# Kernel tuning notes

Hardware: AMD Instinct MI355X
Metric: run time of the kernel (lower is better)

## Reference

```python
import jax, jax.numpy as jnp
import numpy as np

P = 1024          # nodes per graph
B = 64            # graphs in batch
N = P * B         # total nodes
E = N * 32        # total edges (avg degree 32)
D_IN = 16         # per-node feature dim (share_obs_dim)
H = 32            # GCN / MLP hidden dim (hardcoded in GNet)
SHARE = 64        # flat share_state dim


def setup_inputs() -> dict:
    key = jax.random.key(0)
    ks = jax.random.split(key, 20)

    x = jax.random.normal(ks[0], (N, D_IN), jnp.float32)
    src = jax.random.randint(ks[1], (E,), 0, N, dtype=jnp.int32)
    # keep edges inside each 1024-node graph block (PyG batched graphs)
    dst = (src // P) * P + jax.random.randint(ks[2], (E,), 0, P, dtype=jnp.int32)
    edge_index = jnp.stack([src, dst])
    value_batch = (jnp.arange(N, dtype=jnp.int32) // P)
    share_state = jax.random.normal(ks[3], (B, SHARE), jnp.float32)

    def lin(k, o, i):
        return jax.random.normal(k, (o, i), jnp.float32) / np.float32(np.sqrt(i))

    return {
        "x": x, "edge_index": edge_index, "value_batch": value_batch,
        "share_state": share_state,
        # value_gnet: GCNConv(D_IN,32), GCNConv(32,32), Linear(32,32), post-pool Linear(32,32)
        "W1": lin(ks[4], H, D_IN), "b1": jnp.zeros((H,), jnp.float32),
        "W2": lin(ks[5], H, H),    "b2": jnp.zeros((H,), jnp.float32),
        "Wl": lin(ks[6], H, H),    "bl": jnp.zeros((H,), jnp.float32),
        "Wp": lin(ks[7], H, H),    "bp": jnp.zeros((H,), jnp.float32),
        # value_net MLP: SHARE->32->32->32
        "Vw1": lin(ks[8], H, SHARE), "Vb1": jnp.zeros((H,), jnp.float32),
        "Vw2": lin(ks[9], H, H),     "Vb2": jnp.zeros((H,), jnp.float32),
        "Vw3": lin(ks[10], H, H),    "Vb3": jnp.zeros((H,), jnp.float32),
        # value_comnet: 64->32->1
        "Cw1": lin(ks[11], H, 2 * H), "Cb1": jnp.zeros((H,), jnp.float32),
        "Cw2": lin(ks[12], 1, H) * np.float32(0.01), "Cb2": jnp.zeros((1,), jnp.float32),
    }


def gcn_conv(x, src, dst, W, b):
    """PyG GCNConv: D^-1/2 (A+I) D^-1/2 X W^T + b (unit edge weights)."""
    n = x.shape[0]
    loop = jnp.arange(n, dtype=src.dtype)
    s = jnp.concatenate([src, loop])
    d = jnp.concatenate([dst, loop])
    deg = jax.ops.segment_sum(jnp.ones(s.shape[0], x.dtype), d, num_segments=n)
    dis = jnp.where(deg > 0, jax.lax.rsqrt(jnp.maximum(deg, 1e-12)), 0.0)
    norm = dis[s] * dis[d]                      # [E+N]
    h = x @ W.T                                  # [N, H] small GEMM first
    out = jax.ops.segment_sum(h[s] * norm[:, None], d, num_segments=n)
    return out + b


def reference(x, edge_index, value_batch, share_state,
              W1, b1, W2, b2, Wl, bl, Wp, bp,
              Vw1, Vb1, Vw2, Vb2, Vw3, Vb3,
              Cw1, Cb1, Cw2, Cb2):
    src, dst = edge_index[0], edge_index[1]
    nb = share_state.shape[0]

    # value_gnet
    h = jnp.tanh(gcn_conv(x, src, dst, W1, b1))
    h = jnp.tanh(gcn_conv(h, src, dst, W2, b2))
    h = jnp.tanh(h @ Wl.T + bl)
    pooled = jax.ops.segment_sum(h, value_batch, num_segments=nb)  # global_add_pool -> [B, 32]
    h1 = pooled @ Wp.T + bp

    # value_net MLP on flat share_state
    h2 = jnp.tanh(share_state @ Vw1.T + Vb1)
    h2 = jnp.tanh(h2 @ Vw2.T + Vb2)
    h2 = h2 @ Vw3.T + Vb3

    # value_comnet
    z = jnp.tanh(jnp.concatenate([h1, h2], axis=-1) @ Cw1.T + Cb1)
    value = z @ Cw2.T + Cb2                      # [B, 1]
    return value
```

## Files before the change

kernel.cpp:

```cpp
#include <hip/hip_runtime.h>
#include <math.h>

#define NNODES 65536
#define NEDGES 2097152
#define PGRAPH 1024
#define NGRAPH 64
#define CAPB   9216
#define CAPQ   9728

#define OFF_GFILL 0u
#define OFF_ARR   1024u
#define OFF_POOL4 2048u
#define OFF_DIS   34816u
#define OFF_EBUF  296960u
#define OFF_H1G   9734144u

__device__ __forceinline__ float ftanh(float x) {
    float e = __expf(2.f * x);
    return 1.f - 2.f * __builtin_amdgcn_rcpf(e + 1.f);
}

__global__ __launch_bounds__(1024) void k_bucket(
        const int* __restrict__ src, const int* __restrict__ dst,
        int* __restrict__ gfill, unsigned int* __restrict__ ebuf) {
    __shared__ unsigned int sorted[8192];
    __shared__ int hist[256], lexcl[256], gbase[256], lfill[256];
    __shared__ int wsum[4];
    int t = threadIdx.x;
    int blk = blockIdx.x;
    int lane = t & 63, wid = t >> 6;

    if (t < 256) { hist[t] = 0; lfill[t] = 0; }
    __syncthreads();

    unsigned int pk[8];
    {
        const int4* s4p = (const int4*)(src + blk * 8192);
        const int4* d4p = (const int4*)(dst + blk * 8192);
        #pragma unroll
        for (int k = 0; k < 2; k++) {
            int4 s4 = s4p[k * 1024 + t];
            int4 d4 = d4p[k * 1024 + t];
            int ss[4] = { s4.x, s4.y, s4.z, s4.w };
            int dd[4] = { d4.x, d4.y, d4.z, d4.w };
            #pragma unroll
            for (int j = 0; j < 4; j++) {
                int gg = ss[j] >> 10;
                pk[k * 4 + j] = (unsigned int)((ss[j] & 1023) | ((dd[j] & 1023) << 10) | (gg << 20));
                atomicAdd(&hist[(gg << 2) | ((dd[j] >> 8) & 3)], 1);
            }
        }
    }
    __syncthreads();

    int hA = 0, xxA = 0;
    if (t < 256) {
        hA = hist[t];
        xxA = hA;
        #pragma unroll
        for (int off = 1; off < 64; off <<= 1) {
            int y = __shfl_up(xxA, off, 64);
            if (lane >= off) xxA += y;
        }
        if (lane == 63) wsum[wid] = xxA;
    }
    __syncthreads();
    if (t < 256) {
        int pre = 0;
        for (int w = 0; w < wid; w++) pre += wsum[w];
        lexcl[t] = pre + xxA - hA;
        gbase[t] = atomicAdd(&gfill[t], hA);
    }
    __syncthreads();

    #pragma unroll
    for (int k = 0; k < 8; k++) {
        int b = pk[k] >> 18;
        int pos = lexcl[b] + atomicAdd(&lfill[b], 1);
        sorted[pos] = pk[k];
    }
    __syncthreads();
    #pragma unroll
    for (int k = 0; k < 8; k++) {
        int i = k * 1024 + t;
        unsigned int p = sorted[i];
        int b = p >> 18;
        ebuf[(size_t)b * CAPB + gbase[b] + (i - lexcl[b])] = p;
    }
}

__global__ __launch_bounds__(1024, 1) void k_gcn(
        const float* __restrict__ x,
        const float* __restrict__ W1, const float* __restrict__ b1,
        const float* __restrict__ W2, const float* __restrict__ b2,
        const float* __restrict__ Wl, const float* __restrict__ bl,
        const float* __restrict__ Wp, const float* __restrict__ bp,
        const float* __restrict__ Vw1, const float* __restrict__ Vb1,
        const float* __restrict__ Vw2, const float* __restrict__ Vb2,
        const float* __restrict__ Vw3, const float* __restrict__ Vb3,
        const float* __restrict__ Cw1, const float* __restrict__ Cb1,
        const float* __restrict__ Cw2, const float* __restrict__ Cb2,
        const float* __restrict__ share,
        const unsigned int* __restrict__ ebuf, const int* __restrict__ gfill,
        float* __restrict__ disg, float* __restrict__ h1g,
        int* __restrict__ arrive, float* __restrict__ pooled4,
        float* __restrict__ out) {
    __shared__ float hsL[1025 * 32];
    __shared__ unsigned short lcsr[CAPQ];
    __shared__ float WlL[32 * 33];
    __shared__ int hist[256], lrow[256], lfill[256];
    __shared__ int wsum[4];
    float4* hsL4 = (float4*)hsL;

    int t = threadIdx.x;
    int g = blockIdx.x & 63, part = blockIdx.x >> 6;
    int bkt = (g << 2) | part;
    int cnt = gfill[bkt];
    const unsigned int* eb = ebuf + (size_t)bkt * CAPB;

    float inr[16];
    {
        const float4* in4 = (const float4*)(x + ((size_t)(g << 10) + t) * 16);
        #pragma unroll
        for (int k = 0; k < 4; k++) {
            float4 v = in4[k];
            inr[4*k] = v.x; inr[4*k+1] = v.y; inr[4*k+2] = v.z; inr[4*k+3] = v.w;
        }
    }

    if (t < 256) hist[t] = 0;
    WlL[(t >> 5) * 33 + (t & 31)] = Wl[t];
    if (t < 32) hsL[1024 * 32 + t] = 0.f;
    __syncthreads();

    for (int i = t; i < cnt; i += 1024) atomicAdd(&hist[(eb[i] >> 10) & 255], 1);
    __syncthreads();

    int dq = 0, r4 = 0;
    if (t < 256) {
        dq = hist[t]; r4 = (dq + 3) & ~3;
        disg[(g << 10) + part * 256 + t] = rsqrtf((float)(dq + 1));
    }
    __syncthreads();
    if (t == 0)
        __hip_atomic_fetch_add(arrive + g, 1, __ATOMIC_RELEASE, __HIP_MEMORY_SCOPE_AGENT);

    int lane = t & 63, wid = t >> 6;
    int xx = r4;
    #pragma unroll
    for (int off = 1; off < 64; off <<= 1) {
        int y = __shfl_up(xx, off, 64);
        if (lane >= off) xx += y;
    }
    if (t < 256 && lane == 63) wsum[wid] = xx;
    __syncthreads();
    if (t < 256) {
        int pre = 0;
        for (int w = 0; w < wid; w++) pre += wsum[w];
        lrow[t] = pre + xx - r4;
        lfill[t] = 0;
    }
    __syncthreads();

    for (int i = t; i < cnt; i += 1024) {
        unsigned int v = eb[i];
        int dl = (v >> 10) & 255;
        int pos = lrow[dl] + atomicAdd(&lfill[dl], 1);
        lcsr[pos] = (unsigned short)(v & 1023);
    }
    if (t < 256) {
        int st = lrow[t];
        for (int i = dq; i < r4; i++) lcsr[st + i] = 1024;
    }

    if (t == 0) {
        while (__hip_atomic_load(arrive + g, __ATOMIC_RELAXED, __HIP_MEMORY_SCOPE_AGENT) < 4) {}
        (void)__hip_atomic_load(arrive + g, __ATOMIC_ACQUIRE, __HIP_MEMORY_SCOPE_AGENT);
    }
    __syncthreads();

    float dis_t = disg[(g << 10) + t];
    int sw = t & 7;

    #pragma unroll
    for (int o4 = 0; o4 < 8; o4++) {
        float r[4];
        #pragma unroll
        for (int j = 0; j < 4; j++) {
            int o = o4 * 4 + j;
            float s = 0.f;
            #pragma unroll
            for (int k = 0; k < 16; k++) s += inr[k] * W1[o * 16 + k];
            r[j] = s * dis_t;
        }
        hsL4[t * 8 + (o4 ^ sw)] = make_float4(r[0], r[1], r[2], r[3]);
    }
    __syncthreads();

    int q = t & 7, grp = t >> 3;
    #pragma unroll
    for (int pass = 0; pass < 2; pass++) {
        int lq = pass * 128 + grp;
        int ln = part * 256 + lq;
        int d = hist[lq];
        float dn = rsqrtf((float)(d + 1));
        int st = lrow[lq];
        float4 acc = hsL4[ln * 8 + (q ^ (ln & 7))];
        const ushort4* c4 = (const ushort4*)(lcsr + st);
        int d4 = (d + 3) >> 2;
        for (int i = 0; i < d4; i++) {
            ushort4 ss = c4[i];
            float4 v0 = hsL4[ss.x * 8 + (q ^ (ss.x & 7))];
            float4 v1 = hsL4[ss.y * 8 + (q ^ (ss.y & 7))];
            float4 v2 = hsL4[ss.z * 8 + (q ^ (ss.z & 7))];
            float4 v3 = hsL4[ss.w * 8 + (q ^ (ss.w & 7))];
            acc.x += (v0.x + v1.x) + (v2.x + v3.x);
            acc.y += (v0.y + v1.y) + (v2.y + v3.y);
            acc.z += (v0.z + v1.z) + (v2.z + v3.z);
            acc.w += (v0.w + v1.w) + (v2.w + v3.w);
        }
        float4 bb = ((const float4*)b1)[q];
        float4 r;
        r.x = ftanh(dn * acc.x + bb.x);
        r.y = ftanh(dn * acc.y + bb.y);
        r.z = ftanh(dn * acc.z + bb.z);
        r.w = ftanh(dn * acc.w + bb.w);
        ((float4*)h1g)[((size_t)(g << 10) + ln) * 8 + q] = r;
    }
    __syncthreads();
    if (t == 0) {
        __hip_atomic_fetch_add(arrive + 64 + g, 1, __ATOMIC_RELEASE, __HIP_MEMORY_SCOPE_AGENT);
        while (__hip_atomic_load(arrive + 64 + g, __ATOMIC_RELAXED, __HIP_MEMORY_SCOPE_AGENT) < 4) {}
        (void)__hip_atomic_load(arrive + 64 + g, __ATOMIC_ACQUIRE, __HIP_MEMORY_SCOPE_AGENT);
    }
    __syncthreads();

    float r2[32];
    {
        const float4* h4 = (const float4*)(h1g + ((size_t)(g << 10) + t) * 32);
        #pragma unroll
        for (int k = 0; k < 8; k++) {
            float4 v = h4[k];
            r2[4*k] = v.x; r2[4*k+1] = v.y; r2[4*k+2] = v.z; r2[4*k+3] = v.w;
        }
    }
    #pragma unroll
    for (int o4 = 0; o4 < 8; o4++) {
        float r[4];
        #pragma unroll
        for (int j = 0; j < 4; j++) {
            int o = o4 * 4 + j;
            float s = 0.f;
            #pragma unroll
            for (int k = 0; k < 32; k++) s += r2[k] * W2[o * 32 + k];
            r[j] = s * dis_t;
        }
        hsL4[t * 8 + (o4 ^ sw)] = make_float4(r[0], r[1], r[2], r[3]);
    }
    __syncthreads();

    float4 racc[2];
    #pragma unroll
    for (int pass = 0; pass < 2; pass++) {
        int lq = pass * 128 + grp;
        int ln = part * 256 + lq;
        int d = hist[lq];
        float dn = rsqrtf((float)(d + 1));
        int st = lrow[lq];
        float4 acc = hsL4[ln * 8 + (q ^ (ln & 7))];
        const ushort4* c4 = (const ushort4*)(lcsr + st);
        int d4 = (d + 3) >> 2;
        for (int i = 0; i < d4; i++) {
            ushort4 ss = c4[i];
            float4 v0 = hsL4[ss.x * 8 + (q ^ (ss.x & 7))];
            float4 v1 = hsL4[ss.y * 8 + (q ^ (ss.y & 7))];
            float4 v2 = hsL4[ss.z * 8 + (q ^ (ss.z & 7))];
            float4 v3 = hsL4[ss.w * 8 + (q ^ (ss.w & 7))];
            acc.x += (v0.x + v1.x) + (v2.x + v3.x);
            acc.y += (v0.y + v1.y) + (v2.y + v3.y);
            acc.z += (v0.z + v1.z) + (v2.z + v3.z);
            acc.w += (v0.w + v1.w) + (v2.w + v3.w);
        }
        float4 bb = ((const float4*)b2)[q];
        float4 r;
        r.x = ftanh(dn * acc.x + bb.x);
        r.y = ftanh(dn * acc.y + bb.y);
        r.z = ftanh(dn * acc.z + bb.z);
        r.w = ftanh(dn * acc.w + bb.w);
        racc[pass] = r;
    }

    __syncthreads();
    #pragma unroll
    for (int pass = 0; pass < 2; pass++) {
        int lnn = pass * 128 + grp;
        hsL4[lnn * 8 + (q ^ (lnn & 7))] = racc[pass];
    }
    __syncthreads();
    int o = t & 31, seg = t >> 5;
    float ps = 0.f;
    #pragma unroll
    for (int j = 0; j < 8; j++) {
        int nl = seg * 8 + j;
        int swn = nl & 7;
        float s = bl[o];
        #pragma unroll
        for (int k = 0; k < 32; k++) {
            float h2v = hsL[nl * 32 + ((((k >> 2) ^ swn) << 2) | (k & 3))];
            s += h2v * WlL[o * 33 + k];
        }
        ps += ftanh(s);
    }
    float* psum = hsL + 8192;
    psum[t] = ps;
    __syncthreads();
    if (t < 32) {
        float tot = 0.f;
        for (int s = 0; s < 32; s++) tot += psum[s * 32 + t];
        pooled4[(g * 4 + part) * 32 + t] = tot;
    }
    __syncthreads();
    if (t == 0)
        __hip_atomic_fetch_add(arrive + 128 + g, 1, __ATOMIC_RELEASE, __HIP_MEMORY_SCOPE_AGENT);

    if (part == 0) {
        if (t == 0) {
            while (__hip_atomic_load(arrive + 128 + g, __ATOMIC_RELAXED, __HIP_MEMORY_SCOPE_AGENT) < 4) {}
            (void)__hip_atomic_load(arrive + 128 + g, __ATOMIC_ACQUIRE, __HIP_MEMORY_SCOPE_AGENT);
        }
        __syncthreads();
        if (t < 32) {
            int j = t;
            float p = pooled4[(g * 4 + 0) * 32 + j] + pooled4[(g * 4 + 1) * 32 + j]
                    + pooled4[(g * 4 + 2) * 32 + j] + pooled4[(g * 4 + 3) * 32 + j];
            float h1v = bp[j];
            #pragma unroll
            for (int k = 0; k < 32; k++) h1v += Wp[j * 32 + k] * __shfl(p, k, 32);
            float s0 = share[g * 64 + j];
            float s1 = share[g * 64 + 32 + j];
            float t1 = Vb1[j];
            #pragma unroll
            for (int k = 0; k < 32; k++) {
                t1 += Vw1[j * 64 + k] * __shfl(s0, k, 32);
                t1 += Vw1[j * 64 + 32 + k] * __shfl(s1, k, 32);
            }
            t1 = tanhf(t1);
            float t2 = Vb2[j];
            #pragma unroll
            for (int k = 0; k < 32; k++) t2 += Vw2[j * 32 + k] * __shfl(t1, k, 32);
            t2 = tanhf(t2);
            float h2v = Vb3[j];
            #pragma unroll
            for (int k = 0; k < 32; k++) h2v += Vw3[j * 32 + k] * __shfl(t2, k, 32);
            float z = Cb1[j];
            #pragma unroll
            for (int k = 0; k < 32; k++) {
                z += Cw1[j * 64 + k] * __shfl(h1v, k, 32);
                z += Cw1[j * 64 + 32 + k] * __shfl(h2v, k, 32);
            }
            z = tanhf(z);
            float v = Cw2[j] * z;
            v += __shfl_down(v, 16, 32); v += __shfl_down(v, 8, 32);
            v += __shfl_down(v, 4, 32);  v += __shfl_down(v, 2, 32);
            v += __shfl_down(v, 1, 32);
            if (j == 0) out[g] = v + Cb2[0];
        }
    }
}

extern "C" void kernel_launch(void* const* d_in, const int* in_sizes, int n_in,
                              void* d_out, int out_size, void* d_ws, size_t ws_size,
                              hipStream_t stream) {
    const float* x     = (const float*)d_in[0];
    const int*   ei    = (const int*)d_in[1];
    const float* share = (const float*)d_in[3];
    const float* W1 = (const float*)d_in[4];  const float* b1 = (const float*)d_in[5];
    const float* W2 = (const float*)d_in[6];  const float* b2 = (const float*)d_in[7];
    const float* Wl = (const float*)d_in[8];  const float* bl = (const float*)d_in[9];
    const float* Wp = (const float*)d_in[10]; const float* bp = (const float*)d_in[11];
    const float* Vw1 = (const float*)d_in[12]; const float* Vb1 = (const float*)d_in[13];
    const float* Vw2 = (const float*)d_in[14]; const float* Vb2 = (const float*)d_in[15];
    const float* Vw3 = (const float*)d_in[16]; const float* Vb3 = (const float*)d_in[17];
    const float* Cw1 = (const float*)d_in[18]; const float* Cb1 = (const float*)d_in[19];
    const float* Cw2 = (const float*)d_in[20]; const float* Cb2 = (const float*)d_in[21];

    char* ws = (char*)d_ws;
    int*          gfill   = (int*)(ws + OFF_GFILL);
    int*          arrive  = (int*)(ws + OFF_ARR);
    float*        pooled4 = (float*)(ws + OFF_POOL4);
    float*        disg    = (float*)(ws + OFF_DIS);
    unsigned int* ebuf    = (unsigned int*)(ws + OFF_EBUF);
    float*        h1g     = (float*)(ws + OFF_H1G);

    const int* srcp = ei;
    const int* dstp = ei + NEDGES;

    hipMemsetAsync(ws, 0, 2048, stream);

    k_bucket<<<256, 1024, 0, stream>>>(srcp, dstp, gfill, ebuf);
    k_gcn<<<256, 1024, 0, stream>>>(x, W1, b1, W2, b2, Wl, bl, Wp, bp,
                                    Vw1, Vb1, Vw2, Vb2, Vw3, Vb3,
                                    Cw1, Cb1, Cw2, Cb2, share,
                                    ebuf, gfill, disg, h1g, arrive, pooled4,
                                    (float*)d_out);
}
```

Before: 176.7 us.

## Compute node degrees with global atomics in bucketing kernel, drop cross-block degree barrier

Node in-degrees are now counted in the bucketing kernel with global atomicAdd per edge into a zeroed workspace array. The GCN kernel reads these degrees directly, so it no longer needs its own histogram pass over the edge bucket or the inter-block spin barrier that shared the per-part normalisation factors. The cost is two million global atomics in the first kernel and a larger memset.

Result: slower. 254.2 us (+43.9%).

```diff
diff --git a/kernel.cpp b/kernel.cpp
--- a/kernel.cpp
+++ b/kernel.cpp
@@ -3,15 +3,13 @@
 
 #define NNODES 65536
 #define NEDGES 2097152
-#define PGRAPH 1024
-#define NGRAPH 64
 #define CAPB   9216
 #define CAPQ   9728
 
 #define OFF_GFILL 0u
 #define OFF_ARR   1024u
-#define OFF_POOL4 2048u
-#define OFF_DIS   34816u
+#define OFF_DEG   2048u
+#define OFF_POOL4 264192u
 #define OFF_EBUF  296960u
 #define OFF_H1G   9734144u
 
@@ -22,7 +20,8 @@
 
 __global__ __launch_bounds__(1024) void k_bucket(
         const int* __restrict__ src, const int* __restrict__ dst,
-        int* __restrict__ gfill, unsigned int* __restrict__ ebuf) {
+        int* __restrict__ gfill, unsigned int* __restrict__ ebuf,
+        int* __restrict__ deg) {
     __shared__ unsigned int sorted[8192];
     __shared__ int hist[256], lexcl[256], gbase[256], lfill[256];
     __shared__ int wsum[4];
@@ -48,6 +47,7 @@
                 int gg = ss[j] >> 10;
                 pk[k * 4 + j] = (unsigned int)((ss[j] & 1023) | ((dd[j] & 1023) << 10) | (gg << 20));
                 atomicAdd(&hist[(gg << 2) | ((dd[j] >> 8) & 3)], 1);
+                atomicAdd(&deg[dd[j]], 1);
             }
         }
     }
@@ -102,13 +102,13 @@
         const float* __restrict__ Cw2, const float* __restrict__ Cb2,
         const float* __restrict__ share,
         const unsigned int* __restrict__ ebuf, const int* __restrict__ gfill,
-        float* __restrict__ disg, float* __restrict__ h1g,
+        const int* __restrict__ deg, float* __restrict__ h1g,
         int* __restrict__ arrive, float* __restrict__ pooled4,
         float* __restrict__ out) {
     __shared__ float hsL[1025 * 32];
     __shared__ unsigned short lcsr[CAPQ];
     __shared__ float WlL[32 * 33];
-    __shared__ int hist[256], lrow[256], lfill[256];
+    __shared__ int ldeg[256], lrow[256], lfill[256];
     __shared__ int wsum[4];
     float4* hsL4 = (float4*)hsL;
 
@@ -127,24 +127,15 @@
             inr[4*k] = v.x; inr[4*k+1] = v.y; inr[4*k+2] = v.z; inr[4*k+3] = v.w;
         }
     }
-
-    if (t < 256) hist[t] = 0;
+    int deg_own = deg[(g << 10) + t];
+
+    if (t < 256) ldeg[t] = deg[(g << 10) + part * 256 + t];
     WlL[(t >> 5) * 33 + (t & 31)] = Wl[t];
     if (t < 32) hsL[1024 * 32 + t] = 0.f;
     __syncthreads();
 
-    for (int i = t; i < cnt; i += 1024) atomicAdd(&hist[(eb[i] >> 10) & 255], 1);
-    __syncthreads();
-
     int dq = 0, r4 = 0;
-    if (t < 256) {
-        dq = hist[t]; r4 = (dq + 3) & ~3;
-        disg[(g << 10) + part * 256 + t] = rsqrtf((float)(dq + 1));
-    }
-    __syncthreads();
-    if (t == 0)
-        __hip_atomic_fetch_add(arrive + g, 1, __ATOMIC_RELEASE, __HIP_MEMORY_SCOPE_AGENT);
-
+    if (t < 256) { dq = ldeg[t]; r4 = (dq + 3) & ~3; }
     int lane = t & 63, wid = t >> 6;
     int xx = r4;
     #pragma unroll
@@ -173,13 +164,7 @@
         for (int i = dq; i < r4; i++) lcsr[st + i] = 1024;
     }
 
-    if (t == 0) {
-        while (__hip_atomic_load(arrive + g, __ATOMIC_RELAXED, __HIP_MEMORY_SCOPE_AGENT) < 4) {}
-        (void)__hip_atomic_load(arrive + g, __ATOMIC_ACQUIRE, __HIP_MEMORY_SCOPE_AGENT);
-    }
-    __syncthreads();
-
-    float dis_t = disg[(g << 10) + t];
+    float dis_t = rsqrtf((float)(deg_own + 1));
     int sw = t & 7;
 
     #pragma unroll
@@ -202,7 +187,7 @@
     for (int pass = 0; pass < 2; pass++) {
         int lq = pass * 128 + grp;
         int ln = part * 256 + lq;
-        int d = hist[lq];
+        int d = ldeg[lq];
         float dn = rsqrtf((float)(d + 1));
         int st = lrow[lq];
         float4 acc = hsL4[ln * 8 + (q ^ (ln & 7))];
@@ -229,9 +214,9 @@
     }
     __syncthreads();
     if (t == 0) {
-        __hip_atomic_fetch_add(arrive + 64 + g, 1, __ATOMIC_RELEASE, __HIP_MEMORY_SCOPE_AGENT);
-        while (__hip_atomic_load(arrive + 64 + g, __ATOMIC_RELAXED, __HIP_MEMORY_SCOPE_AGENT) < 4) {}
-        (void)__hip_atomic_load(arrive + 64 + g, __ATOMIC_ACQUIRE, __HIP_MEMORY_SCOPE_AGENT);
+        __hip_atomic_fetch_add(arrive + g, 1, __ATOMIC_RELEASE, __HIP_MEMORY_SCOPE_AGENT);
+        while (__hip_atomic_load(arrive + g, __ATOMIC_RELAXED, __HIP_MEMORY_SCOPE_AGENT) < 4) {}
+        (void)__hip_atomic_load(arrive + g, __ATOMIC_ACQUIRE, __HIP_MEMORY_SCOPE_AGENT);
     }
     __syncthreads();
 
@@ -264,7 +249,7 @@
     for (int pass = 0; pass < 2; pass++) {
         int lq = pass * 128 + grp;
         int ln = part * 256 + lq;
-        int d = hist[lq];
+        int d = ldeg[lq];
         float dn = rsqrtf((float)(d + 1));
         int st = lrow[lq];
         float4 acc = hsL4[ln * 8 + (q ^ (ln & 7))];
@@ -321,12 +306,12 @@
     }
     __syncthreads();
     if (t == 0)
-        __hip_atomic_fetch_add(arrive + 128 + g, 1, __ATOMIC_RELEASE, __HIP_MEMORY_SCOPE_AGENT);
+        __hip_atomic_fetch_add(arrive + 64 + g, 1, __ATOMIC_RELEASE, __HIP_MEMORY_SCOPE_AGENT);
 
     if (part == 0) {
         if (t == 0) {
-            while (__hip_atomic_load(arrive + 128 + g, __ATOMIC_RELAXED, __HIP_MEMORY_SCOPE_AGENT) < 4) {}
-            (void)__hip_atomic_load(arrive + 128 + g, __ATOMIC_ACQUIRE, __HIP_MEMORY_SCOPE_AGENT);
+            while (__hip_atomic_load(arrive + 64 + g, __ATOMIC_RELAXED, __HIP_MEMORY_SCOPE_AGENT) < 4) {}
+            (void)__hip_atomic_load(arrive + 64 + g, __ATOMIC_ACQUIRE, __HIP_MEMORY_SCOPE_AGENT);
         }
         __syncthreads();
         if (t < 32) {
@@ -387,20 +372,20 @@
     char* ws = (char*)d_ws;
     int*          gfill   = (int*)(ws + OFF_GFILL);
     int*          arrive  = (int*)(ws + OFF_ARR);
+    int*          deg     = (int*)(ws + OFF_DEG);
     float*        pooled4 = (float*)(ws + OFF_POOL4);
-    float*        disg    = (float*)(ws + OFF_DIS);
     unsigned int* ebuf    = (unsigned int*)(ws + OFF_EBUF);
     float*        h1g     = (float*)(ws + OFF_H1G);
 
     const int* srcp = ei;
     const int* dstp = ei + NEDGES;
 
-    hipMemsetAsync(ws, 0, 2048, stream);
-
-    k_bucket<<<256, 1024, 0, stream>>>(srcp, dstp, gfill, ebuf);
+    hipMemsetAsync(ws, 0, 264192, stream);
+
+    k_bucket<<<256, 1024, 0, stream>>>(srcp, dstp, gfill, ebuf, deg);
     k_gcn<<<256, 1024, 0, stream>>>(x, W1, b1, W2, b2, Wl, bl, Wp, bp,
                                     Vw1, Vb1, Vw2, Vb2, Vw3, Vb3,
                                     Cw1, Cb1, Cw2, Cb2, share,
-                                    ebuf, gfill, disg, h1g, arrive, pooled4,
+                                    ebuf, gfill, deg, h1g, arrive, pooled4,
                                     (float*)d_out);
 }
```
